# Optimization experiments

Measured on AMD Instinct MI355X. Metric: run time of the kernel, lower is better.

Reference implementation:

```python
import jax, jax.numpy as jnp
import numpy as np

B, N, E, H = 16, 768, 1024, 16  # batch == heads so mask[i] (head-indexed, as in the source) is valid
D = E // H
MASK_P = 0.1
NEG = jnp.float32(-1e16)


def setup_inputs() -> dict:
    key = jax.random.key(0)
    ks = jax.random.split(key, 8)
    query = jax.random.normal(ks[0], (B, N, E), jnp.float32)
    key_t = jax.random.normal(ks[1], (B, N, E), jnp.float32)
    value = jax.random.normal(ks[2], (B, N, E), jnp.float32)
    u = jax.random.uniform(ks[3], (B, N))
    mask = jnp.where(u < MASK_P, -jnp.inf, 0.0).astype(jnp.float32)
    # per-head Linear(head_dim, head_dim, bias=False) weights, stacked over heads: (H, out=D, in=D)
    Wq = jax.random.normal(ks[4], (H, D, D), jnp.float32) * (1.0 / np.sqrt(D))
    Wk = jax.random.normal(ks[5], (H, D, D), jnp.float32) * (1.0 / np.sqrt(D))
    Wv = jax.random.normal(ks[6], (H, D, D), jnp.float32) * (1.0 / np.sqrt(D))
    Wf = jax.random.normal(ks[7], (E, E), jnp.float32) * (1.0 / np.sqrt(E))
    return {"query": query, "key": key_t, "value": value, "mask": mask,
            "Wq": Wq, "Wk": Wk, "Wv": Wv, "Wf": Wf}


def reference(query, key, value, mask, Wq, Wk, Wv, Wf):
    b, n, e = query.shape
    h = Wq.shape[0]
    d = e // h
    q = query.reshape(b, n, h, d)
    k = key.reshape(b, n, h, d)
    v = value.reshape(b, n, h, d)
    # per-head nn.Linear: x @ W[i].T  (W: (H, out, in))
    qh = jnp.einsum('bnhd,hed->bnhe', q, Wq)
    kh = jnp.einsum('bnhd,hed->bnhe', k, Wk)
    vh = jnp.einsum('bnhd,hed->bnhe', v, Wv)
    # scaled QK^T: divide by embed_size**0.5 (NOT head_dim) as in the source
    scores = jnp.einsum('bqhd,bkhd->bhqk', qh, kh) / jnp.sqrt(jnp.float32(e))  # (B,H,N,N)
    # faithful quirk: mask row selected by HEAD index i -> same additive mask for all batches
    bad = jnp.isneginf(mask)[:h]                      # (H, N)
    add = jnp.where(bad[:, :, None] | bad[:, None, :], NEG, jnp.float32(0.0))  # (H,N,N): row/col blanked
    probs = jax.nn.softmax(scores + add[None], axis=-1)
    attn = jnp.einsum('bhqk,bkhd->bqhd', probs, vh)   # (B,N,H,D)
    out = attn.reshape(b, n, e) @ Wf.T
    return out
```

## Files before the change

### kernel.cpp

```cpp
#include <hip/hip_runtime.h>

#define B_ 16
#define N_ 768
#define E_ 1024
#define H_ 16
#define D_ 64

typedef __bf16 bf16x8 __attribute__((ext_vector_type(8)));
typedef float f32x4 __attribute__((ext_vector_type(4)));
typedef unsigned short ushort8 __attribute__((ext_vector_type(8)));
typedef unsigned short ushort4v __attribute__((ext_vector_type(4)));
typedef unsigned int uint2v __attribute__((ext_vector_type(2)));
typedef unsigned int uint4v __attribute__((ext_vector_type(4)));

__device__ __forceinline__ unsigned short f2bf(float x) {
  unsigned u = __builtin_bit_cast(unsigned, x);
  u += 0x7FFFu + ((u >> 16) & 1u);
  return (unsigned short)(u >> 16);
}

__device__ __forceinline__ unsigned cvtpk(float lo, float hi) {
  unsigned r;
  asm("v_cvt_pk_bf16_f32 %0, %1, %2" : "=v"(r) : "v"(lo), "v"(hi));
  return r;
}

__device__ __forceinline__ float fexp2(float x) {
  float r;
  asm("v_exp_f32 %0, %1" : "=v"(r) : "v"(x));
  return r;
}

__device__ __forceinline__ f32x4 mfma16(ushort8 a, ushort8 b, f32x4 c) {
  return __builtin_amdgcn_mfma_f32_16x16x32_bf16(
      __builtin_bit_cast(bf16x8, a), __builtin_bit_cast(bf16x8, b), c, 0, 0, 0);
}

#define GLD16(gsrc, ldst)                                              \
  __builtin_amdgcn_global_load_lds(                                   \
      (const __attribute__((address_space(1))) void*)(gsrc),          \
      (__attribute__((address_space(3))) void*)(ldst), 16, 0, 0)

__global__ __launch_bounds__(256) void proj_kernel(
    const float* __restrict__ q, const float* __restrict__ k, const float* __restrict__ v,
    const float* __restrict__ Wq, const float* __restrict__ Wk, const float* __restrict__ Wv,
    const float* __restrict__ Wf, unsigned short* __restrict__ Qh,
    unsigned short* __restrict__ Kh, unsigned short* __restrict__ Vt,
    unsigned short* __restrict__ Wfb) {
  const int m = blockIdx.x / 3072;
  const int rest = blockIdx.x - m * 3072;
  const int nt = rest % 12;
  const int bh = rest / 12;
  const int b = bh >> 4, h = bh & 15;
  const int tid = threadIdx.x;
  const int w = tid >> 6, l = tid & 63;
  const int l16 = l & 15, lg = l >> 4;

  if (blockIdx.x < 1024) {
    size_t g = (size_t)blockIdx.x * 256 + tid;
    float4 xv = *(const float4*)&Wf[g * 4];
    ushort4v s;
    s[0] = f2bf(xv.x); s[1] = f2bf(xv.y); s[2] = f2bf(xv.z); s[3] = f2bf(xv.w);
    *(ushort4v*)&Wfb[g * 4] = s;
  }

  __shared__ __align__(16) unsigned short Xs[64][72];
  __shared__ __align__(16) unsigned short Ws[64][72];

  const float* xp = (m == 0) ? q : (m == 1) ? k : v;
  const float* wp = ((m == 0) ? Wq : (m == 1) ? Wk : Wv) + (size_t)h * 4096;

#pragma unroll
  for (int i = 0; i < 4; ++i) {
    int flat = i * 256 + tid;
    int row = flat >> 4;
    int c4 = (flat & 15) * 4;
    float4 xv = *(const float4*)&xp[((size_t)(b * N_ + nt * 64 + row)) * E_ + h * 64 + c4];
    ushort4v s;
    s[0] = f2bf(xv.x); s[1] = f2bf(xv.y); s[2] = f2bf(xv.z); s[3] = f2bf(xv.w);
    *(ushort4v*)&Xs[row][c4] = s;
  }
#pragma unroll
  for (int i = 0; i < 4; ++i) {
    int flat = i * 256 + tid;
    int row = flat >> 4;
    int c4 = (flat & 15) * 4;
    float4 wv = *(const float4*)&wp[row * 64 + c4];
    ushort4v s;
    s[0] = f2bf(wv.x); s[1] = f2bf(wv.y); s[2] = f2bf(wv.z); s[3] = f2bf(wv.w);
    *(ushort4v*)&Ws[row][c4] = s;
  }
  __syncthreads();

  f32x4 acc[4] = {};
#pragma unroll
  for (int kc = 0; kc < 2; ++kc) {
    ushort8 a = *(const ushort8*)&Xs[w * 16 + l16][kc * 32 + lg * 8];
#pragma unroll
    for (int eg = 0; eg < 4; ++eg) {
      ushort8 bf = *(const ushort8*)&Ws[eg * 16 + l16][kc * 32 + lg * 8];
      acc[eg] = mfma16(a, bf, acc[eg]);
    }
  }

  if (m < 2) {
    unsigned short* op = (m == 0) ? Qh : Kh;
    __syncthreads();
#pragma unroll
    for (int eg = 0; eg < 4; ++eg)
#pragma unroll
      for (int r = 0; r < 4; ++r)
        Xs[w * 16 + lg * 4 + r][eg * 16 + l16] = f2bf(acc[eg][r]);
    __syncthreads();
#pragma unroll
    for (int i = 0; i < 2; ++i) {
      int row = i * 32 + (tid >> 3), c8 = (tid & 7) * 8;
      *(ushort8*)&op[((size_t)(b * H_ + h) * N_ + nt * 64 + row) * 64 + c8] =
          *(const ushort8*)&Xs[row][c8];
    }
  } else {
    __syncthreads();
#pragma unroll
    for (int eg = 0; eg < 4; ++eg) {
      uint2v pk;
      pk[0] = cvtpk(acc[eg][0], acc[eg][1]);
      pk[1] = cvtpk(acc[eg][2], acc[eg][3]);
      *(uint2v*)&Xs[eg * 16 + l16][w * 16 + lg * 4] = pk;
    }
    __syncthreads();
#pragma unroll
    for (int i = 0; i < 2; ++i) {
      int row = i * 32 + (tid >> 3), c8 = (tid & 7) * 8;
      *(ushort8*)&Vt[((size_t)bh * 64 + row) * N_ + nt * 64 + c8] =
          *(const ushort8*)&Xs[row][c8];
    }
  }
}

__global__ __launch_bounds__(256, 4) void attn_kernel(
    const unsigned short* __restrict__ Qh, const unsigned short* __restrict__ Kh,
    const unsigned short* __restrict__ Vt, const float* __restrict__ mask,
    unsigned short* __restrict__ attnO) {
  const int bid = blockIdx.x;
  const int logical = (bid & 7) * 192 + (bid >> 3);
  const int qt = logical % 6;
  const int bh = logical / 6;
  const int b = bh >> 4, h = bh & 15;
  const int tid = threadIdx.x;
  const int w = tid >> 6, l = tid & 63;
  const int l16 = l & 15, lg = l >> 4;

  __shared__ __align__(16) unsigned short Ks[64][72];
  __shared__ __align__(16) unsigned short Vs[64][72];
  __shared__ __align__(16) unsigned short Ps[4][32][72];
  __shared__ float addk[N_];

  const size_t baseK = (size_t)bh * N_ * 64;
  const size_t baseV = (size_t)bh * 64 * N_;
  const int qrow0 = qt * 128 + w * 32;
  const float C2 = 0.04508422f;

  for (int i = tid; i < N_; i += 256)
    addk[i] = (mask[h * N_ + i] < -1e30f) ? -1.0e20f : 0.0f;

  ushort8 bQ[2][2];
#pragma unroll
  for (int qs = 0; qs < 2; ++qs)
#pragma unroll
    for (int kc = 0; kc < 2; ++kc)
      bQ[qs][kc] = *(const ushort8*)&Qh[((size_t)bh * N_ + qrow0 + qs * 16 + l16) * 64 +
                                        kc * 32 + lg * 8];
  float bqf[2];
#pragma unroll
  for (int qs = 0; qs < 2; ++qs)
    bqf[qs] = (mask[h * N_ + qrow0 + qs * 16 + l16] < -1e30f) ? 1.f : 0.f;

  const int srow = tid >> 3;
  const int sc8 = (tid & 7) * 8;

  uint4v kreg[2], vreg[2];
#pragma unroll
  for (int i = 0; i < 2; ++i) {
    int row = i * 32 + srow;
    kreg[i] = *(const uint4v*)&Kh[baseK + (size_t)row * 64 + sc8];
    vreg[i] = *(const uint4v*)&Vt[baseV + (size_t)row * N_ + sc8];
  }
  __syncthreads();
#pragma unroll
  for (int i = 0; i < 2; ++i) {
    int row = i * 32 + srow;
    *(ushort8*)&Ks[row][sc8] = __builtin_bit_cast(ushort8, kreg[i]);
    *(ushort8*)&Vs[row][sc8] = __builtin_bit_cast(ushort8, vreg[i]);
  }
  __syncthreads();

  f32x4 oacc[2][4] = {};
  float l_part[2] = {0.f, 0.f};

  for (int kt = 0; kt < 12; ++kt) {
    if (kt < 11) {
#pragma unroll
      for (int i = 0; i < 2; ++i) {
        int row = i * 32 + srow;
        kreg[i] = *(const uint4v*)&Kh[baseK + (size_t)((kt + 1) * 64 + row) * 64 + sc8];
        vreg[i] = *(const uint4v*)&Vt[baseV + (size_t)row * N_ + (kt + 1) * 64 + sc8];
      }
    }

#pragma unroll
    for (int cg = 0; cg < 4; ++cg) {
      f32x4 st[2] = {};
#pragma unroll
      for (int kc = 0; kc < 2; ++kc) {
        ushort8 aK = *(const ushort8*)&Ks[cg * 16 + l16][kc * 32 + lg * 8];
        st[0] = mfma16(aK, bQ[0][kc], st[0]);
        st[1] = mfma16(aK, bQ[1][kc], st[1]);
      }
      f32x4 ak4 = *(const f32x4*)&addk[kt * 64 + cg * 16 + lg * 4];
#pragma unroll
      for (int qs = 0; qs < 2; ++qs) {
        float p[4];
#pragma unroll
        for (int r = 0; r < 4; ++r) {
          float t = __builtin_fmaf(st[qs][r], C2, ak4[r]);
          t = (bqf[qs] > 0.f) ? 0.0f : t;
          p[r] = fexp2(t);
          l_part[qs] += p[r];
        }
        uint2v pk;
        pk[0] = cvtpk(p[0], p[1]);
        pk[1] = cvtpk(p[2], p[3]);
        *(uint2v*)&Ps[w][qs * 16 + l16][cg * 16 + lg * 4] = pk;
      }
    }

#pragma unroll
    for (int kc = 0; kc < 2; ++kc) {
      ushort8 ap[2];
#pragma unroll
      for (int qs = 0; qs < 2; ++qs)
        ap[qs] = *(const ushort8*)&Ps[w][qs * 16 + l16][kc * 32 + lg * 8];
#pragma unroll
      for (int dg = 0; dg < 4; ++dg) {
        ushort8 bv = *(const ushort8*)&Vs[dg * 16 + l16][kc * 32 + lg * 8];
        oacc[0][dg] = mfma16(ap[0], bv, oacc[0][dg]);
        oacc[1][dg] = mfma16(ap[1], bv, oacc[1][dg]);
      }
    }

    __syncthreads();
    if (kt < 11) {
#pragma unroll
      for (int i = 0; i < 2; ++i) {
        int row = i * 32 + srow;
        *(ushort8*)&Ks[row][sc8] = __builtin_bit_cast(ushort8, kreg[i]);
        *(ushort8*)&Vs[row][sc8] = __builtin_bit_cast(ushort8, vreg[i]);
      }
    }
    __syncthreads();
  }

#pragma unroll
  for (int qs = 0; qs < 2; ++qs) {
    float s = l_part[qs];
    s += __shfl_xor(s, 16);
    s += __shfl_xor(s, 32);
#pragma unroll
    for (int r = 0; r < 4; ++r) {
      float dnm = __shfl(s, lg * 4 + r);
      float inv = 1.f / dnm;
      int qg = qrow0 + qs * 16 + lg * 4 + r;
      size_t orow = ((size_t)b * N_ + qg) * E_ + h * 64;
#pragma unroll
      for (int dg = 0; dg < 4; ++dg)
        attnO[orow + dg * 16 + l16] = f2bf(oacc[qs][dg][r] * inv);
    }
  }
}

__global__ __launch_bounds__(256) void gemm_kernel(const unsigned short* __restrict__ A,
                                                   const unsigned short* __restrict__ Bm,
                                                   float* __restrict__ out) {
  const int be = blockIdx.x & 7;
  const int bm = blockIdx.x >> 3;
  const int tid = threadIdx.x;
  const int w = tid >> 6, l = tid & 63;
  const int l16 = l & 15, lg = l >> 4;
  const int wm = w >> 1, wn = w & 1;

  __shared__ __align__(16) unsigned short As[128 * 64];
  __shared__ __align__(16) unsigned short Bs[128 * 64];

  const int m0 = bm * 128, e0 = be * 128;

  const int srow8 = l >> 3;
  const int scol = (l & 7) * 8;
  const unsigned short* gA[4];
  const unsigned short* gB[4];
#pragma unroll
  for (int j = 0; j < 4; ++j) {
    int tr = (w * 4 + j) * 8 + srow8;
    gA[j] = A + (size_t)(m0 + tr) * E_ + scol;
    gB[j] = Bm + (size_t)(e0 + tr) * E_ + scol;
  }

  f32x4 acc[4][4] = {};

  for (int kk = 0; kk < 16; ++kk) {
    __syncthreads();
#pragma unroll
    for (int j = 0; j < 4; ++j) {
      int ch = w * 4 + j;
      GLD16(gA[j] + kk * 64, (char*)As + ch * 1024);
      GLD16(gB[j] + kk * 64, (char*)Bs + ch * 1024);
    }
    asm volatile("s_waitcnt vmcnt(0)" ::: "memory");
    __syncthreads();

#pragma unroll
    for (int kc = 0; kc < 2; ++kc) {
      ushort8 a[4], bf[4];
#pragma unroll
      for (int i = 0; i < 4; ++i)
        a[i] = *(const ushort8*)&As[(wm * 64 + i * 16 + l16) * 64 + kc * 32 + lg * 8];
#pragma unroll
      for (int j = 0; j < 4; ++j)
        bf[j] = *(const ushort8*)&Bs[(wn * 64 + j * 16 + l16) * 64 + kc * 32 + lg * 8];
#pragma unroll
      for (int i = 0; i < 4; ++i)
#pragma unroll
        for (int j = 0; j < 4; ++j) acc[i][j] = mfma16(a[i], bf[j], acc[i][j]);
    }
  }

#pragma unroll
  for (int i = 0; i < 4; ++i)
#pragma unroll
    for (int j = 0; j < 4; ++j)
#pragma unroll
      for (int r = 0; r < 4; ++r)
        out[(size_t)(m0 + wm * 64 + i * 16 + lg * 4 + r) * E_ + e0 + wn * 64 + j * 16 + l16] =
            acc[i][j][r];
}

extern "C" void kernel_launch(void* const* d_in, const int* in_sizes, int n_in,
                              void* d_out, int out_size, void* d_ws, size_t ws_size,
                              hipStream_t stream) {
  const float* q = (const float*)d_in[0];
  const float* k = (const float*)d_in[1];
  const float* v = (const float*)d_in[2];
  const float* mask = (const float*)d_in[3];
  const float* Wq = (const float*)d_in[4];
  const float* Wk = (const float*)d_in[5];
  const float* Wv = (const float*)d_in[6];
  const float* Wf = (const float*)d_in[7];
  float* out = (float*)d_out;

  const size_t PH = (size_t)B_ * H_ * N_ * D_;
  unsigned short* Qh = (unsigned short*)d_ws;
  unsigned short* Kh = Qh + PH;
  unsigned short* Vt = Kh + PH;
  unsigned short* attn = Vt + PH;
  unsigned short* Wfb = attn + PH;

  proj_kernel<<<3 * B_ * H_ * (N_ / 64), 256, 0, stream>>>(q, k, v, Wq, Wk, Wv, Wf, Qh, Kh,
                                                           Vt, Wfb);
  attn_kernel<<<B_ * H_ * (N_ / 128), 256, 0, stream>>>(Qh, Kh, Vt, mask, attn);
  gemm_kernel<<<(B_ * N_ / 128) * (E_ / 128), 256, 0, stream>>>(attn, Wfb, out);
}
```

Measured before the change: 158.0 us.

## Register-prefetch GEMM tiles into padded LDS and batch projection loads early

The output GEMM stops using direct global-to-LDS loads with a full vmcnt wait. It now loads the next K tile into registers while MFMAs run on the current tile, then stores to LDS padded to 72 columns to avoid bank conflicts. The projection kernel issues all its X, W and Wf global loads up front before any conversion, so more memory requests are in flight. The cost is higher register pressure, extra LDS store instructions, and a launch bound of one block per SIMD hint on the projection kernel.

```diff
diff --git a/kernel.cpp b/kernel.cpp
--- a/kernel.cpp
+++ b/kernel.cpp
@@ -36,12 +36,7 @@
       __builtin_bit_cast(bf16x8, a), __builtin_bit_cast(bf16x8, b), c, 0, 0, 0);
 }
 
-#define GLD16(gsrc, ldst)                                              \
-  __builtin_amdgcn_global_load_lds(                                   \
-      (const __attribute__((address_space(1))) void*)(gsrc),          \
-      (__attribute__((address_space(3))) void*)(ldst), 16, 0, 0)
-
-__global__ __launch_bounds__(256) void proj_kernel(
+__global__ __launch_bounds__(256, 1) void proj_kernel(
     const float* __restrict__ q, const float* __restrict__ k, const float* __restrict__ v,
     const float* __restrict__ Wq, const float* __restrict__ Wk, const float* __restrict__ Wv,
     const float* __restrict__ Wf, unsigned short* __restrict__ Qh,
@@ -56,39 +51,43 @@
   const int w = tid >> 6, l = tid & 63;
   const int l16 = l & 15, lg = l >> 4;
 
-  if (blockIdx.x < 1024) {
-    size_t g = (size_t)blockIdx.x * 256 + tid;
-    float4 xv = *(const float4*)&Wf[g * 4];
-    ushort4v s;
-    s[0] = f2bf(xv.x); s[1] = f2bf(xv.y); s[2] = f2bf(xv.z); s[3] = f2bf(xv.w);
-    *(ushort4v*)&Wfb[g * 4] = s;
-  }
-
   __shared__ __align__(16) unsigned short Xs[64][72];
   __shared__ __align__(16) unsigned short Ws[64][72];
 
   const float* xp = (m == 0) ? q : (m == 1) ? k : v;
   const float* wp = ((m == 0) ? Wq : (m == 1) ? Wk : Wv) + (size_t)h * 4096;
 
+  const int row = tid >> 4;
+  const int c4 = (tid & 15) * 4;
+
+  float4 xt[4], wt[4];
+#pragma unroll
+  for (int i = 0; i < 4; ++i)
+    xt[i] = *(const float4*)&xp[((size_t)(b * N_ + nt * 64 + i * 16 + row)) * E_ + h * 64 + c4];
+#pragma unroll
+  for (int i = 0; i < 4; ++i)
+    wt[i] = *(const float4*)&wp[(i * 16 + row) * 64 + c4];
+
+  float4 wfv;
+  if (blockIdx.x < 1024)
+    wfv = *(const float4*)&Wf[((size_t)blockIdx.x * 256 + tid) * 4];
+
 #pragma unroll
   for (int i = 0; i < 4; ++i) {
-    int flat = i * 256 + tid;
-    int row = flat >> 4;
-    int c4 = (flat & 15) * 4;
-    float4 xv = *(const float4*)&xp[((size_t)(b * N_ + nt * 64 + row)) * E_ + h * 64 + c4];
     ushort4v s;
-    s[0] = f2bf(xv.x); s[1] = f2bf(xv.y); s[2] = f2bf(xv.z); s[3] = f2bf(xv.w);
-    *(ushort4v*)&Xs[row][c4] = s;
+    s[0] = f2bf(xt[i].x); s[1] = f2bf(xt[i].y); s[2] = f2bf(xt[i].z); s[3] = f2bf(xt[i].w);
+    *(ushort4v*)&Xs[i * 16 + row][c4] = s;
   }
 #pragma unroll
   for (int i = 0; i < 4; ++i) {
-    int flat = i * 256 + tid;
-    int row = flat >> 4;
-    int c4 = (flat & 15) * 4;
-    float4 wv = *(const float4*)&wp[row * 64 + c4];
     ushort4v s;
-    s[0] = f2bf(wv.x); s[1] = f2bf(wv.y); s[2] = f2bf(wv.z); s[3] = f2bf(wv.w);
-    *(ushort4v*)&Ws[row][c4] = s;
+    s[0] = f2bf(wt[i].x); s[1] = f2bf(wt[i].y); s[2] = f2bf(wt[i].z); s[3] = f2bf(wt[i].w);
+    *(ushort4v*)&Ws[i * 16 + row][c4] = s;
+  }
+  if (blockIdx.x < 1024) {
+    ushort4v s;
+    s[0] = f2bf(wfv.x); s[1] = f2bf(wfv.y); s[2] = f2bf(wfv.z); s[3] = f2bf(wfv.w);
+    *(ushort4v*)&Wfb[((size_t)blockIdx.x * 256 + tid) * 4] = s;
   }
   __syncthreads();
 
@@ -114,9 +113,9 @@
     __syncthreads();
 #pragma unroll
     for (int i = 0; i < 2; ++i) {
-      int row = i * 32 + (tid >> 3), c8 = (tid & 7) * 8;
-      *(ushort8*)&op[((size_t)(b * H_ + h) * N_ + nt * 64 + row) * 64 + c8] =
-          *(const ushort8*)&Xs[row][c8];
+      int rw = i * 32 + (tid >> 3), c8 = (tid & 7) * 8;
+      *(ushort8*)&op[((size_t)(b * H_ + h) * N_ + nt * 64 + rw) * 64 + c8] =
+          *(const ushort8*)&Xs[rw][c8];
     }
   } else {
     __syncthreads();
@@ -130,9 +129,9 @@
     __syncthreads();
 #pragma unroll
     for (int i = 0; i < 2; ++i) {
-      int row = i * 32 + (tid >> 3), c8 = (tid & 7) * 8;
-      *(ushort8*)&Vt[((size_t)bh * 64 + row) * N_ + nt * 64 + c8] =
-          *(const ushort8*)&Xs[row][c8];
+      int rw = i * 32 + (tid >> 3), c8 = (tid & 7) * 8;
+      *(ushort8*)&Vt[((size_t)bh * 64 + rw) * N_ + nt * 64 + c8] =
+          *(const ushort8*)&Xs[rw][c8];
     }
   }
 }
@@ -288,44 +287,46 @@
   const int l16 = l & 15, lg = l >> 4;
   const int wm = w >> 1, wn = w & 1;
 
-  __shared__ __align__(16) unsigned short As[128 * 64];
-  __shared__ __align__(16) unsigned short Bs[128 * 64];
-
+  __shared__ __align__(16) unsigned short As[128][72];
+  __shared__ __align__(16) unsigned short Bs[128][72];
+
+  f32x4 acc[4][4] = {};
   const int m0 = bm * 128, e0 = be * 128;
-
-  const int srow8 = l >> 3;
-  const int scol = (l & 7) * 8;
-  const unsigned short* gA[4];
-  const unsigned short* gB[4];
-#pragma unroll
-  for (int j = 0; j < 4; ++j) {
-    int tr = (w * 4 + j) * 8 + srow8;
-    gA[j] = A + (size_t)(m0 + tr) * E_ + scol;
-    gB[j] = Bm + (size_t)(e0 + tr) * E_ + scol;
-  }
-
-  f32x4 acc[4][4] = {};
+  const int srow = tid >> 3, sc8 = (tid & 7) * 8;
+  const unsigned short* Ab = A + (size_t)(m0 + srow) * E_ + sc8;
+  const unsigned short* Bb = Bm + (size_t)(e0 + srow) * E_ + sc8;
+
+  uint4v ar[4], br[4];
+#pragma unroll
+  for (int i = 0; i < 4; ++i) {
+    ar[i] = *(const uint4v*)(Ab + (size_t)i * 32 * E_);
+    br[i] = *(const uint4v*)(Bb + (size_t)i * 32 * E_);
+  }
 
   for (int kk = 0; kk < 16; ++kk) {
     __syncthreads();
 #pragma unroll
-    for (int j = 0; j < 4; ++j) {
-      int ch = w * 4 + j;
-      GLD16(gA[j] + kk * 64, (char*)As + ch * 1024);
-      GLD16(gB[j] + kk * 64, (char*)Bs + ch * 1024);
-    }
-    asm volatile("s_waitcnt vmcnt(0)" ::: "memory");
-    __syncthreads();
-
+    for (int i = 0; i < 4; ++i) {
+      *(ushort8*)&As[i * 32 + srow][sc8] = __builtin_bit_cast(ushort8, ar[i]);
+      *(ushort8*)&Bs[i * 32 + srow][sc8] = __builtin_bit_cast(ushort8, br[i]);
+    }
+    __syncthreads();
+    if (kk < 15) {
+#pragma unroll
+      for (int i = 0; i < 4; ++i) {
+        ar[i] = *(const uint4v*)(Ab + (size_t)i * 32 * E_ + (kk + 1) * 64);
+        br[i] = *(const uint4v*)(Bb + (size_t)i * 32 * E_ + (kk + 1) * 64);
+      }
+    }
 #pragma unroll
     for (int kc = 0; kc < 2; ++kc) {
       ushort8 a[4], bf[4];
 #pragma unroll
       for (int i = 0; i < 4; ++i)
-        a[i] = *(const ushort8*)&As[(wm * 64 + i * 16 + l16) * 64 + kc * 32 + lg * 8];
+        a[i] = *(const ushort8*)&As[wm * 64 + i * 16 + l16][kc * 32 + lg * 8];
 #pragma unroll
       for (int j = 0; j < 4; ++j)
-        bf[j] = *(const ushort8*)&Bs[(wn * 64 + j * 16 + l16) * 64 + kc * 32 + lg * 8];
+        bf[j] = *(const ushort8*)&Bs[wn * 64 + j * 16 + l16][kc * 32 + lg * 8];
 #pragma unroll
       for (int i = 0; i < 4; ++i)
 #pragma unroll
```

Result: faster. 140.8 us (-10.9%).
